# Performance work log

Measured on AMD Instinct MI355X. Metric: run time of the kernel, lower is better.

The kernel has to match this reference:

```python
import jax, jax.numpy as jnp
import numpy as np

NUM_NODES = 8192
MUL = 64
ENV_P = 6
EPSILON = 1.0 / np.sqrt(17.0)  # 1/sqrt(1 + avg_num_neighbors), avg_num_neighbors=16


def _envelope(u, p=ENV_P):
    # polynomial smoothing envelope (cutoff at u = 1)
    a = -(p + 1) * (p + 2) / 2.0
    b = p * (p + 2)
    c = -p * (p + 1) / 2.0
    f = 1.0 + a * u ** p + b * u ** (p + 1) + c * u ** (p + 2)
    return jnp.where(u < 1.0, f, 0.0)


def setup_inputs() -> dict:
    key = jax.random.key(0)
    ks = jax.random.split(key, 9)
    E, F = 131072, 512
    vectors = jax.random.normal(ks[0], (E, 3), jnp.float32) * 0.35  # mostly inside cutoff
    x = jax.random.normal(ks[1], (E, F), jnp.float32)
    V = jax.random.normal(ks[2], (E, MUL, 4), jnp.float32)  # per mul-channel: [0e | 1o(3)]
    senders = jax.random.randint(ks[3], (E,), 0, NUM_NODES, jnp.int32)
    W_w = jax.random.normal(ks[4], (F, MUL), jnp.float32)
    W1 = jax.random.normal(ks[5], (F + 2 * MUL, 512), jnp.float32)
    W2 = jax.random.normal(ks[6], (512, 512), jnp.float32)
    W3 = jax.random.normal(ks[7], (512, 512), jnp.float32)
    W_lin = jax.random.normal(ks[8], (3 * MUL, MUL), jnp.float32)
    return {"vectors": vectors, "x": x, "V": V, "senders": senders,
            "W_w": W_w, "W1": W1, "W2": W2, "W3": W3, "W_lin": W_lin}


def reference(vectors, x, V, senders, W_w, W1, W2, W3, W_lin):
    E = vectors.shape[0]
    # edge-wise linear producing tensor-product weights  [E, MUL]
    w = (x @ W_w) / np.sqrt(x.shape[-1])
    # spherical harmonics (component norm), l = 0..1 of normalized vectors -> [E, 4]
    r = jnp.linalg.norm(vectors, axis=-1, keepdims=True)          # [E, 1]
    nhat = vectors / r
    Y = jnp.concatenate([jnp.ones((E, 1), vectors.dtype), np.sqrt(3.0) * nhat], axis=1)
    # weighted SH, scatter-sum over senders, gather back (map_back=True), scale by epsilon
    wY_e = w[:, :, None] * Y[:, None, :]                          # [E, MUL, 4]
    agg = jax.ops.segment_sum(wY_e, senders, num_segments=NUM_NODES)
    wY = agg[senders] * EPSILON                                   # [E, MUL, 4]
    # CG tensor product wY (0e+1o) x V (0e+1o), keep 0e and 1o outputs
    a0, a1 = wY[..., 0], wY[..., 1:]
    b0, b1 = V[..., 0], V[..., 1:]
    scal = jnp.concatenate(
        [a0 * b0, jnp.einsum('emi,emi->em', a1, b1) / np.sqrt(3.0)], axis=-1)  # [E, 2*MUL]
    vecs = jnp.concatenate(
        [a0[..., None] * b1, a1 * b0[..., None], jnp.cross(a1, b1) / np.sqrt(2.0)],
        axis=1)                                                   # [E, 3*MUL, 3]
    # concat scalar channel into invariants, 3-layer MLP (silu, linear last)
    xc = jnp.concatenate([x, scal], axis=1)                       # [E, 640]
    h = jax.nn.silu(xc @ W1 / np.sqrt(xc.shape[-1]))
    h = jax.nn.silu(h @ W2 / np.sqrt(h.shape[-1]))
    h = h @ W3 / np.sqrt(h.shape[-1])
    x_out = _envelope(r) * h                                      # [E, 512]
    # equivariant linear over the 1o multiplicity axis
    V_out = jnp.einsum('ekc,km->emc', vecs, W_lin) / np.sqrt(vecs.shape[1])  # [E, MUL, 3]
    return x_out, V_out
```

## Files before the change

kernel.cpp:

```cpp
#include <hip/hip_runtime.h>
#include <cstdint>
#include <cstddef>

#define E_TOT 131072
#define NNODES 8192

typedef __attribute__((ext_vector_type(8))) short bf16x8;
typedef __attribute__((ext_vector_type(4))) float f32x4;
typedef unsigned short u16;
typedef unsigned int u32;

__device__ __forceinline__ u16 f2bf(float f) {
    u32 u = __builtin_bit_cast(u32, f);
    u32 r = (u + 0x7FFFu + ((u >> 16) & 1u)) >> 16;
    return (u16)r;
}

__device__ __forceinline__ void gload16(const u16* g, u16* l) {
    __builtin_amdgcn_global_load_lds((const __attribute__((address_space(1))) void*)g,
                                     (__attribute__((address_space(3))) void*)l, 16, 0, 0);
}

__device__ __forceinline__ bf16x8 lds_frag(const u16* base, int row, int bytecol) {
    return *(const bf16x8*)((const char*)base + row * 128 + (bytecol ^ ((row & 7) << 4)));
}

__global__ void wconv_kernel(const float* __restrict__ src, u16* __restrict__ dst,
                             int K, int N) {
    int idx = blockIdx.x * 256 + threadIdx.x;
    if (idx >= N * K) return;
    int n = idx / K, k = idx - n * K;
    dst[idx] = f2bf(src[(size_t)k * N + n]);
}

__global__ void xconv_kernel(const float4* __restrict__ x, ushort4* __restrict__ xb) {
    size_t i = (size_t)blockIdx.x * 256 + threadIdx.x;
    float4 v = x[i];
    ushort4 o;
    o.x = f2bf(v.x); o.y = f2bf(v.y); o.z = f2bf(v.z); o.w = f2bf(v.w);
    xb[i] = o;
}

__global__ void envy_kernel(const float* __restrict__ vectors, float* __restrict__ env,
                            float4* __restrict__ Y) {
    int e = blockIdx.x * 256 + threadIdx.x;
    float vx = vectors[3 * e + 0], vy = vectors[3 * e + 1], vz = vectors[3 * e + 2];
    float r2 = vx * vx + vy * vy + vz * vz;
    float r = sqrtf(r2);
    float u6 = r2 * r2 * r2;
    float f = 1.0f + u6 * (-28.0f + 48.0f * r - 21.0f * r2);
    env[e] = (r < 1.0f) ? f : 0.0f;
    float inv = 1.7320508075688772f / r;
    Y[e] = make_float4(1.0f, vx * inv, vy * inv, vz * inv);
}

__global__ void hist_kernel(const int* __restrict__ senders, int* __restrict__ cnt) {
    int e = blockIdx.x * 256 + threadIdx.x;
    atomicAdd(&cnt[senders[e]], 1);
}

__launch_bounds__(1024)
__global__ void scan_kernel(const int* __restrict__ cnt, int* __restrict__ off,
                            int* __restrict__ curs) {
    __shared__ int part[1024];
    const int t = threadIdx.x;
    int local[8];
    int s = 0;
#pragma unroll
    for (int j = 0; j < 8; ++j) { local[j] = cnt[t * 8 + j]; s += local[j]; }
    part[t] = s;
    __syncthreads();
    for (int d = 1; d < 1024; d <<= 1) {
        int v = (t >= d) ? part[t - d] : 0;
        __syncthreads();
        part[t] += v;
        __syncthreads();
    }
    int run = part[t] - s;
#pragma unroll
    for (int j = 0; j < 8; ++j) {
        off[t * 8 + j] = run;
        curs[t * 8 + j] = run;
        run += local[j];
    }
    if (t == 1023) off[8192] = run;
}

__global__ void permbuild_kernel(const int* __restrict__ senders, int* __restrict__ curs,
                                 int* __restrict__ perm) {
    int e = blockIdx.x * 256 + threadIdx.x;
    int s = senders[e];
    int p = atomicAdd(&curs[s], 1);
    perm[p] = e;
}

__launch_bounds__(256)
__global__ void gather_kernel(const float* __restrict__ w, const float4* __restrict__ Y,
                              const int* __restrict__ off, const int* __restrict__ perm,
                              float4* __restrict__ agg) {
    const int t = threadIdx.x;
    const int n = blockIdx.x * 4 + (t >> 6);
    const int m = t & 63;
    const int beg = off[n], end = off[n + 1];
    float4 acc = make_float4(0.f, 0.f, 0.f, 0.f);
    for (int i = beg; i < end; ++i) {
        int e = perm[i];
        float wv = w[(size_t)e * 64 + m];
        float4 y = Y[e];
        acc.x += wv * y.x; acc.y += wv * y.y; acc.z += wv * y.z; acc.w += wv * y.w;
    }
    agg[(size_t)n * 64 + m] = acc;
}

__launch_bounds__(256)
__global__ void wgemm_kernel(const u16* __restrict__ XB, const u16* __restrict__ Wt,
                             float* __restrict__ w) {
    __shared__ u16 As[128 * 72];
    __shared__ u16 Bs[64 * 72];
    const int e0 = blockIdx.x * 128;
    const int t = threadIdx.x, lane = t & 63, wid = t >> 6;
    const int lr = lane & 15, lh = lane >> 4;
    const int r8 = t >> 3, c8 = t & 7;
    f32x4 acc[2][4] = {};
    for (int kt = 0; kt < 8; ++kt) {
        const int kk = kt << 6;
#pragma unroll
        for (int i = 0; i < 4; ++i) {
            int row = i * 32 + r8;
            const u16* g = XB + (size_t)(e0 + row) * 512 + kk + c8 * 8;
            *(uint4*)((char*)As + row * 144 + c8 * 16) = *(const uint4*)g;
        }
#pragma unroll
        for (int i = 0; i < 2; ++i) {
            int row = i * 32 + r8;
            const u16* g = Wt + (size_t)row * 512 + kk + c8 * 8;
            *(uint4*)((char*)Bs + row * 144 + c8 * 16) = *(const uint4*)g;
        }
        __syncthreads();
#pragma unroll
        for (int k2 = 0; k2 < 2; ++k2) {
            bf16x8 af[2], bfr[4];
#pragma unroll
            for (int m = 0; m < 2; ++m)
                af[m] = *(const bf16x8*)((const char*)As + (wid * 32 + m * 16 + lr) * 144 + k2 * 64 + lh * 16);
#pragma unroll
            for (int n = 0; n < 4; ++n)
                bfr[n] = *(const bf16x8*)((const char*)Bs + (n * 16 + lr) * 144 + k2 * 64 + lh * 16);
#pragma unroll
            for (int m = 0; m < 2; ++m)
#pragma unroll
                for (int n = 0; n < 4; ++n)
                    acc[m][n] = __builtin_amdgcn_mfma_f32_16x16x32_bf16(af[m], bfr[n], acc[m][n], 0, 0, 0);
        }
        __syncthreads();
    }
    const float s = 0.044194173824159216f;
#pragma unroll
    for (int m = 0; m < 2; ++m)
#pragma unroll
        for (int n = 0; n < 4; ++n)
#pragma unroll
            for (int j = 0; j < 4; ++j) {
                int e = e0 + wid * 32 + m * 16 + lh * 4 + j;
                w[(size_t)e * 64 + n * 16 + lr] = acc[m][n][j] * s;
            }
}

__launch_bounds__(256)
__global__ void edge_kernel(const int* __restrict__ senders, const float4* __restrict__ agg4,
                            const float4* __restrict__ V4, const u16* __restrict__ Wlt,
                            u16* __restrict__ scal, float* __restrict__ Vout) {
    __shared__ u16 a_lds[3][32][200];
    __shared__ u16 w_lds[64 * 200];
    const int t = threadIdx.x;
    const int e0 = blockIdx.x * 32;
#pragma unroll
    for (int i = 0; i < 6; ++i) {
        int c = i * 256 + t;
        int row = c / 24, off = (c % 24) * 8;
        *(uint4*)((char*)w_lds + row * 400 + off * 2) = ((const uint4*)Wlt)[c];
    }
    const float invs3 = 0.5773502691896258f;
    const float invs2 = 0.7071067811865476f;
    const float EPS = 0.24253562503633297f;
#pragma unroll
    for (int i = 0; i < 8; ++i) {
        int el = i * 4 + (t >> 6);
        int m = t & 63;
        int e = e0 + el;
        int s = senders[e];
        float4 a = agg4[(size_t)s * 64 + m];
        a.x *= EPS; a.y *= EPS; a.z *= EPS; a.w *= EPS;
        float4 b = V4[(size_t)e * 64 + m];
        float s0 = a.x * b.x;
        float s1 = (a.y * b.y + a.z * b.z + a.w * b.w) * invs3;
        scal[(size_t)e * 128 + m] = f2bf(s0);
        scal[(size_t)e * 128 + 64 + m] = f2bf(s1);
        float cx = (a.z * b.w - a.w * b.z) * invs2;
        float cy = (a.w * b.y - a.y * b.w) * invs2;
        float cz = (a.y * b.z - a.z * b.y) * invs2;
        a_lds[0][el][m] = f2bf(a.x * b.y);
        a_lds[0][el][64 + m] = f2bf(a.y * b.x);
        a_lds[0][el][128 + m] = f2bf(cx);
        a_lds[1][el][m] = f2bf(a.x * b.z);
        a_lds[1][el][64 + m] = f2bf(a.z * b.x);
        a_lds[1][el][128 + m] = f2bf(cy);
        a_lds[2][el][m] = f2bf(a.x * b.w);
        a_lds[2][el][64 + m] = f2bf(a.w * b.x);
        a_lds[2][el][128 + m] = f2bf(cz);
    }
    __syncthreads();
    const int lane = t & 63, wid = t >> 6;
    const int lr = lane & 15, lh = lane >> 4;
    f32x4 acc[3][2] = {};
    for (int kt = 0; kt < 6; ++kt) {
        bf16x8 bfr = *(const bf16x8*)((const char*)w_lds + (wid * 16 + lr) * 400 + kt * 64 + lh * 16);
#pragma unroll
        for (int c = 0; c < 3; ++c)
#pragma unroll
            for (int m = 0; m < 2; ++m) {
                bf16x8 afr = *(const bf16x8*)((const char*)a_lds + ((c * 32 + m * 16 + lr) * 400) + kt * 64 + lh * 16);
                acc[c][m] = __builtin_amdgcn_mfma_f32_16x16x32_bf16(afr, bfr, acc[c][m], 0, 0, 0);
            }
    }
    __syncthreads();
    float* ot = (float*)a_lds;
    const float sc = 0.07216878364870323f;
#pragma unroll
    for (int c = 0; c < 3; ++c)
#pragma unroll
        for (int m = 0; m < 2; ++m)
#pragma unroll
            for (int j = 0; j < 4; ++j) {
                int row = m * 16 + lh * 4 + j;
                int mul = wid * 16 + lr;
                ot[row * 192 + mul * 3 + c] = acc[c][m][j] * sc;
            }
    __syncthreads();
    float4* vo = (float4*)(Vout + (size_t)e0 * 192);
#pragma unroll
    for (int i = 0; i < 6; ++i)
        vo[i * 256 + t] = ((float4*)ot)[i * 256 + t];
}

template <int MODE>
__launch_bounds__(512, 2)
__global__ void mlp_gemm(const u16* __restrict__ A, const u16* __restrict__ A2,
                         const u16* __restrict__ Bt, const int K, const float scale,
                         const float* __restrict__ env,
                         u16* __restrict__ outb, float* __restrict__ outf) {
    __shared__ u16 lds[2][2][256 * 64];
    const int nwg = gridDim.x;
    const int bid = blockIdx.x;
    const int swz = (bid & 7) * (nwg >> 3) + (bid >> 3);
    const int mt = swz >> 1, nt = swz & 1;
    const int e0 = mt << 8, n0 = nt << 8;
    const int t = threadIdx.x, lane = t & 63, wid = t >> 6;
    const int wm = wid >> 2, wn = wid & 3;
    const int lr = lane & 15, lh = lane >> 4;
    const int sr8 = lane >> 3;
    const int scol = ((lane & 7) ^ sr8) << 3;
    f32x4 acc[8][4] = {};
    const int nkt = K >> 6;

    auto issue = [&](int kt, int b) {
        const int kk = kt << 6;
        const int col = kk + scol;
#pragma unroll
        for (int i = 0; i < 4; ++i) {
            const int row = e0 + i * 64 + wid * 8 + sr8;
            const u16* g;
            if (A2 && kk >= 512) g = A2 + (size_t)row * 128 + (col - 512);
            else                 g = A + (size_t)row * 512 + col;
            gload16(g, (u16*)&lds[b][0][i * 4096 + wid * 512]);
        }
#pragma unroll
        for (int i = 0; i < 4; ++i) {
            const int row = n0 + i * 64 + wid * 8 + sr8;
            gload16(Bt + (size_t)row * K + col, (u16*)&lds[b][1][i * 4096 + wid * 512]);
        }
    };

    issue(0, 0);
    issue(1, 1);
    for (int kt = 0; kt < nkt; ++kt) {
        if (kt + 1 < nkt) asm volatile("s_waitcnt vmcnt(8)\ns_barrier" ::: "memory");
        else              asm volatile("s_waitcnt vmcnt(0)\ns_barrier" ::: "memory");
        const u16* Ab = lds[kt & 1][0];
        const u16* Bb = lds[kt & 1][1];
        __builtin_amdgcn_s_setprio(1);
#pragma unroll
        for (int k2 = 0; k2 < 2; ++k2) {
            bf16x8 af[8], bfr[4];
#pragma unroll
            for (int m = 0; m < 8; ++m)
                af[m] = lds_frag(Ab, wm * 128 + m * 16 + lr, k2 * 64 + lh * 16);
#pragma unroll
            for (int n = 0; n < 4; ++n)
                bfr[n] = lds_frag(Bb, wn * 64 + n * 16 + lr, k2 * 64 + lh * 16);
#pragma unroll
            for (int m = 0; m < 8; ++m)
#pragma unroll
                for (int n = 0; n < 4; ++n)
                    acc[m][n] = __builtin_amdgcn_mfma_f32_16x16x32_bf16(af[m], bfr[n], acc[m][n], 0, 0, 0);
        }
        __builtin_amdgcn_s_setprio(0);
        if (kt + 2 < nkt) {
            asm volatile("s_waitcnt lgkmcnt(0)\ns_barrier" ::: "memory");
            issue(kt + 2, kt & 1);
        }
    }
#pragma unroll
    for (int m = 0; m < 8; ++m) {
#pragma unroll
        for (int j = 0; j < 4; ++j) {
            const int row = e0 + wm * 128 + m * 16 + lh * 4 + j;
            float ev = (MODE == 1) ? env[row] : 0.0f;
#pragma unroll
            for (int n = 0; n < 4; ++n) {
                const int col = n0 + wn * 64 + n * 16 + lr;
                float v = acc[m][n][j] * scale;
                if (MODE == 0) {
                    float sv = v / (1.0f + __expf(-v));
                    outb[(size_t)row * 512 + col] = f2bf(sv);
                } else {
                    outf[(size_t)row * 512 + col] = v * ev;
                }
            }
        }
    }
}

extern "C" void kernel_launch(void* const* d_in, const int* in_sizes, int n_in,
                              void* d_out, int out_size, void* d_ws, size_t ws_size,
                              hipStream_t stream) {
    const float* vectors = (const float*)d_in[0];
    const float* x       = (const float*)d_in[1];
    const float* V       = (const float*)d_in[2];
    const int*   senders = (const int*)d_in[3];
    const float* W_w     = (const float*)d_in[4];
    const float* W1      = (const float*)d_in[5];
    const float* W2      = (const float*)d_in[6];
    const float* W3      = (const float*)d_in[7];
    const float* W_lin   = (const float*)d_in[8];
    float* out = (float*)d_out;
    char* ws = (char*)d_ws;

    u16*    XB   = (u16*)(ws + 0x0);
    u16*    H1   = (u16*)(ws + 0x8000000);
    u16*    SCAL = (u16*)(ws + 0x10000000);
    float*  AGG  = (float*)(ws + 0x12000000);
    float*  ENV  = (float*)(ws + 0x12800000);
    float4* Yb   = (float4*)(ws + 0x12880000);
    float*  Wbuf = (float*)(ws + 0x12A80000);
    u16*    WT   = (u16*)(ws + 0x14A80000);
    u16* Wwt = WT;
    u16* W1t = Wwt + 64 * 512;
    u16* W2t = W1t + 512 * 640;
    u16* W3t = W2t + 512 * 512;
    u16* Wlt = W3t + 512 * 512;
    u16* H2 = XB;
    int* COUNT = (int*)(ws + 0x15000000);
    int* OFF   = (int*)(ws + 0x15010000);
    int* CURS  = (int*)(ws + 0x15020000);
    int* PERM  = (int*)(ws + 0x15030000);

    hipMemsetAsync(COUNT, 0, NNODES * sizeof(int), stream);

    wconv_kernel<<<(64 * 512) / 256, 256, 0, stream>>>(W_w, Wwt, 512, 64);
    wconv_kernel<<<(512 * 640) / 256, 256, 0, stream>>>(W1, W1t, 640, 512);
    wconv_kernel<<<(512 * 512) / 256, 256, 0, stream>>>(W2, W2t, 512, 512);
    wconv_kernel<<<(512 * 512) / 256, 256, 0, stream>>>(W3, W3t, 512, 512);
    wconv_kernel<<<(64 * 192) / 256, 256, 0, stream>>>(W_lin, Wlt, 192, 64);

    xconv_kernel<<<(E_TOT * 512 / 4) / 256, 256, 0, stream>>>((const float4*)x, (ushort4*)XB);
    envy_kernel<<<E_TOT / 256, 256, 0, stream>>>(vectors, ENV, Yb);

    hist_kernel<<<E_TOT / 256, 256, 0, stream>>>(senders, COUNT);
    scan_kernel<<<1, 1024, 0, stream>>>(COUNT, OFF, CURS);
    permbuild_kernel<<<E_TOT / 256, 256, 0, stream>>>(senders, CURS, PERM);

    wgemm_kernel<<<E_TOT / 128, 256, 0, stream>>>(XB, Wwt, Wbuf);
    gather_kernel<<<NNODES / 4, 256, 0, stream>>>(Wbuf, Yb, OFF, PERM, (float4*)AGG);

    edge_kernel<<<E_TOT / 32, 256, 0, stream>>>(senders, (const float4*)AGG, (const float4*)V,
                                                Wlt, SCAL, out + (size_t)E_TOT * 512);

    const float s640 = 0.03952847075210474f;
    const float s512 = 0.044194173824159216f;
    const int gemm_grid = (E_TOT / 256) * 2;
    mlp_gemm<0><<<gemm_grid, 512, 0, stream>>>(XB, SCAL, W1t, 640, s640, nullptr, H1, nullptr);
    mlp_gemm<0><<<gemm_grid, 512, 0, stream>>>(H1, nullptr, W2t, 512, s512, nullptr, H2, nullptr);
    mlp_gemm<1><<<gemm_grid, 512, 0, stream>>>(H2, nullptr, W3t, 512, s512, ENV, nullptr, out);
}
```

Measured before the change: 602.0 us.

## Fuse x bf16 conversion into wgemm and make MLP GEMMs persistent

```diff
diff --git a/kernel.cpp b/kernel.cpp
--- a/kernel.cpp
+++ b/kernel.cpp
@@ -31,14 +31,6 @@
     if (idx >= N * K) return;
     int n = idx / K, k = idx - n * K;
     dst[idx] = f2bf(src[(size_t)k * N + n]);
-}
-
-__global__ void xconv_kernel(const float4* __restrict__ x, ushort4* __restrict__ xb) {
-    size_t i = (size_t)blockIdx.x * 256 + threadIdx.x;
-    float4 v = x[i];
-    ushort4 o;
-    o.x = f2bf(v.x); o.y = f2bf(v.y); o.z = f2bf(v.z); o.w = f2bf(v.w);
-    xb[i] = o;
 }
 
 __global__ void envy_kernel(const float* __restrict__ vectors, float* __restrict__ env,
@@ -113,8 +105,8 @@
 }
 
 __launch_bounds__(256)
-__global__ void wgemm_kernel(const u16* __restrict__ XB, const u16* __restrict__ Wt,
-                             float* __restrict__ w) {
+__global__ void wgemm_kernel(const float* __restrict__ x, const u16* __restrict__ Wt,
+                             u16* __restrict__ XB, float* __restrict__ w) {
     __shared__ u16 As[128 * 72];
     __shared__ u16 Bs[64 * 72];
     const int e0 = blockIdx.x * 128;
@@ -127,8 +119,14 @@
 #pragma unroll
         for (int i = 0; i < 4; ++i) {
             int row = i * 32 + r8;
-            const u16* g = XB + (size_t)(e0 + row) * 512 + kk + c8 * 8;
-            *(uint4*)((char*)As + row * 144 + c8 * 16) = *(const uint4*)g;
+            const float* gx = x + (size_t)(e0 + row) * 512 + kk + c8 * 8;
+            float4 a = *(const float4*)gx;
+            float4 b = *(const float4*)(gx + 4);
+            union { u16 h[8]; uint4 v; } p;
+            p.h[0] = f2bf(a.x); p.h[1] = f2bf(a.y); p.h[2] = f2bf(a.z); p.h[3] = f2bf(a.w);
+            p.h[4] = f2bf(b.x); p.h[5] = f2bf(b.y); p.h[6] = f2bf(b.z); p.h[7] = f2bf(b.w);
+            *(uint4*)((char*)As + row * 144 + c8 * 16) = p.v;
+            *(uint4*)(XB + (size_t)(e0 + row) * 512 + kk + c8 * 8) = p.v;
         }
 #pragma unroll
         for (int i = 0; i < 2; ++i) {
@@ -243,51 +241,57 @@
         vo[i * 256 + t] = ((float4*)ot)[i * 256 + t];
 }
 
-template <int MODE>
+template <int MODE, int K>
 __launch_bounds__(512, 2)
 __global__ void mlp_gemm(const u16* __restrict__ A, const u16* __restrict__ A2,
-                         const u16* __restrict__ Bt, const int K, const float scale,
+                         const u16* __restrict__ Bt, const float scale,
                          const float* __restrict__ env,
                          u16* __restrict__ outb, float* __restrict__ outf) {
+    constexpr int NKT = K >> 6;
+    constexpr int NSTEP = NKT * 4;
     __shared__ u16 lds[2][2][256 * 64];
-    const int nwg = gridDim.x;
-    const int bid = blockIdx.x;
-    const int swz = (bid & 7) * (nwg >> 3) + (bid >> 3);
-    const int mt = swz >> 1, nt = swz & 1;
-    const int e0 = mt << 8, n0 = nt << 8;
+    const int b = blockIdx.x;
     const int t = threadIdx.x, lane = t & 63, wid = t >> 6;
     const int wm = wid >> 2, wn = wid & 3;
     const int lr = lane & 15, lh = lane >> 4;
     const int sr8 = lane >> 3;
     const int scol = ((lane & 7) ^ sr8) << 3;
     f32x4 acc[8][4] = {};
-    const int nkt = K >> 6;
-
-    auto issue = [&](int kt, int b) {
+
+    auto issue = [&](int g) {
+        const int tile = g / NKT;
+        const int kt = g - tile * NKT;
+        const int tid = b * 4 + tile;
+        const int e0 = (tid >> 1) << 8;
+        const int n0 = (tid & 1) << 8;
         const int kk = kt << 6;
         const int col = kk + scol;
+        const int buf = g & 1;
 #pragma unroll
         for (int i = 0; i < 4; ++i) {
             const int row = e0 + i * 64 + wid * 8 + sr8;
-            const u16* g;
-            if (A2 && kk >= 512) g = A2 + (size_t)row * 128 + (col - 512);
-            else                 g = A + (size_t)row * 512 + col;
-            gload16(g, (u16*)&lds[b][0][i * 4096 + wid * 512]);
+            const u16* gp;
+            if (A2 && kk >= 512) gp = A2 + (size_t)row * 128 + (col - 512);
+            else                 gp = A + (size_t)row * 512 + col;
+            gload16(gp, (u16*)&lds[buf][0][i * 4096 + wid * 512]);
         }
 #pragma unroll
         for (int i = 0; i < 4; ++i) {
             const int row = n0 + i * 64 + wid * 8 + sr8;
-            gload16(Bt + (size_t)row * K + col, (u16*)&lds[b][1][i * 4096 + wid * 512]);
+            gload16(Bt + (size_t)row * K + col, (u16*)&lds[buf][1][i * 4096 + wid * 512]);
         }
     };
 
-    issue(0, 0);
-    issue(1, 1);
-    for (int kt = 0; kt < nkt; ++kt) {
-        if (kt + 1 < nkt) asm volatile("s_waitcnt vmcnt(8)\ns_barrier" ::: "memory");
-        else              asm volatile("s_waitcnt vmcnt(0)\ns_barrier" ::: "memory");
-        const u16* Ab = lds[kt & 1][0];
-        const u16* Bb = lds[kt & 1][1];
+    issue(0);
+    issue(1);
+    for (int g = 0; g < NSTEP; ++g) {
+        const int tile = g / NKT;
+        const int kt = g - tile * NKT;
+        if (g + 1 >= NSTEP)           asm volatile("s_waitcnt vmcnt(0)\ns_barrier" ::: "memory");
+        else if (kt <= 1 && tile > 0) asm volatile("s_waitcnt vmcnt(40)\ns_barrier" ::: "memory");
+        else                          asm volatile("s_waitcnt vmcnt(8)\ns_barrier" ::: "memory");
+        const u16* Ab = lds[g & 1][0];
+        const u16* Bb = lds[g & 1][1];
         __builtin_amdgcn_s_setprio(1);
 #pragma unroll
         for (int k2 = 0; k2 < 2; ++k2) {
@@ -305,28 +309,36 @@
                     acc[m][n] = __builtin_amdgcn_mfma_f32_16x16x32_bf16(af[m], bfr[n], acc[m][n], 0, 0, 0);
         }
         __builtin_amdgcn_s_setprio(0);
-        if (kt + 2 < nkt) {
-            asm volatile("s_waitcnt lgkmcnt(0)\ns_barrier" ::: "memory");
-            issue(kt + 2, kt & 1);
-        }
-    }
-#pragma unroll
-    for (int m = 0; m < 8; ++m) {
-#pragma unroll
-        for (int j = 0; j < 4; ++j) {
-            const int row = e0 + wm * 128 + m * 16 + lh * 4 + j;
-            float ev = (MODE == 1) ? env[row] : 0.0f;
-#pragma unroll
-            for (int n = 0; n < 4; ++n) {
-                const int col = n0 + wn * 64 + n * 16 + lr;
-                float v = acc[m][n][j] * scale;
-                if (MODE == 0) {
-                    float sv = v / (1.0f + __expf(-v));
-                    outb[(size_t)row * 512 + col] = f2bf(sv);
-                } else {
-                    outf[(size_t)row * 512 + col] = v * ev;
+        asm volatile("s_waitcnt lgkmcnt(0)\ns_barrier" ::: "memory");
+        if (g + 2 < NSTEP) issue(g + 2);
+        if (kt == NKT - 1) {
+            const int tid = b * 4 + tile;
+            const int e0 = (tid >> 1) << 8;
+            const int n0 = (tid & 1) << 8;
+#pragma unroll
+            for (int m = 0; m < 8; ++m) {
+#pragma unroll
+                for (int j = 0; j < 4; ++j) {
+                    const int row = e0 + wm * 128 + m * 16 + lh * 4 + j;
+                    float ev = (MODE == 1) ? env[row] : 0.0f;
+#pragma unroll
+                    for (int n = 0; n < 4; ++n) {
+                        const int col = n0 + wn * 64 + n * 16 + lr;
+                        float v = acc[m][n][j] * scale;
+                        if (MODE == 0) {
+                            float sv = v / (1.0f + __expf(-v));
+                            outb[(size_t)row * 512 + col] = f2bf(sv);
+                        } else {
+                            outf[(size_t)row * 512 + col] = v * ev;
+                        }
+                    }
                 }
             }
+#pragma unroll
+            for (int m = 0; m < 8; ++m)
+#pragma unroll
+                for (int n = 0; n < 4; ++n)
+                    acc[m][n] = f32x4{0.f, 0.f, 0.f, 0.f};
         }
     }
 }
@@ -373,14 +385,13 @@
     wconv_kernel<<<(512 * 512) / 256, 256, 0, stream>>>(W3, W3t, 512, 512);
     wconv_kernel<<<(64 * 192) / 256, 256, 0, stream>>>(W_lin, Wlt, 192, 64);
 
-    xconv_kernel<<<(E_TOT * 512 / 4) / 256, 256, 0, stream>>>((const float4*)x, (ushort4*)XB);
     envy_kernel<<<E_TOT / 256, 256, 0, stream>>>(vectors, ENV, Yb);
 
     hist_kernel<<<E_TOT / 256, 256, 0, stream>>>(senders, COUNT);
     scan_kernel<<<1, 1024, 0, stream>>>(COUNT, OFF, CURS);
     permbuild_kernel<<<E_TOT / 256, 256, 0, stream>>>(senders, CURS, PERM);
 
-    wgemm_kernel<<<E_TOT / 128, 256, 0, stream>>>(XB, Wwt, Wbuf);
+    wgemm_kernel<<<E_TOT / 128, 256, 0, stream>>>(x, Wwt, XB, Wbuf);
     gather_kernel<<<NNODES / 4, 256, 0, stream>>>(Wbuf, Yb, OFF, PERM, (float4*)AGG);
 
     edge_kernel<<<E_TOT / 32, 256, 0, stream>>>(senders, (const float4*)AGG, (const float4*)V,
@@ -388,8 +399,7 @@
 
     const float s640 = 0.03952847075210474f;
     const float s512 = 0.044194173824159216f;
-    const int gemm_grid = (E_TOT / 256) * 2;
-    mlp_gemm<0><<<gemm_grid, 512, 0, stream>>>(XB, SCAL, W1t, 640, s640, nullptr, H1, nullptr);
-    mlp_gemm<0><<<gemm_grid, 512, 0, stream>>>(H1, nullptr, W2t, 512, s512, nullptr, H2, nullptr);
-    mlp_gemm<1><<<gemm_grid, 512, 0, stream>>>(H2, nullptr, W3t, 512, s512, ENV, nullptr, out);
-}
+    mlp_gemm<0, 640><<<256, 512, 0, stream>>>(XB, SCAL, W1t, s640, nullptr, H1, nullptr);
+    mlp_gemm<0, 512><<<256, 512, 0, stream>>>(H1, nullptr, W2t, s512, nullptr, H2, nullptr);
+    mlp_gemm<1, 512><<<256, 512, 0, stream>>>(H2, nullptr, W3t, s512, ENV, nullptr, out);
+}
```

Measured after the change: 586.5 us. 2.6% less time.
